# Optimization experiments

Hardware: AMD Instinct MI355X
Metric: run time of the kernel (lower is better)

## Reference

```python
import jax, jax.numpy as jnp
import numpy as np

N = 50000          # nodes
E = 800000         # edges (avg degree 16)
IN_FEATS = 128
OUT_FEATS = 64
HEADS = 4
HID = HEADS * OUT_FEATS  # 256
NEG_SLOPE = 0.2          # PyG GATConv default
EPS = 1e-5               # BatchNorm eps


def setup_inputs() -> dict:
    key = jax.random.key(0)
    ks = jax.random.split(key, 8)
    x = jax.random.normal(ks[0], (N, IN_FEATS), dtype=jnp.float32)
    edge_index = jax.random.randint(ks[1], (2, E), 0, N, dtype=jnp.int32)
    edge_attr = jax.random.normal(ks[2], (E, 8), dtype=jnp.float32)  # unused (edge_dim=None)
    # GATConv params
    W_gat = jax.random.normal(ks[3], (IN_FEATS, HEADS, OUT_FEATS), jnp.float32) * (1.0 / np.sqrt(IN_FEATS))
    att_src = jax.random.normal(ks[4], (HEADS, OUT_FEATS), jnp.float32) * 0.1
    att_dst = jax.random.normal(ks[5], (HEADS, OUT_FEATS), jnp.float32) * 0.1
    bias_gat = jnp.zeros((HID,), jnp.float32)
    # BatchNorm1 + Linear + BatchNorm2 params
    bn1_gamma = jnp.ones((HID,), jnp.float32)
    bn1_beta = jnp.zeros((HID,), jnp.float32)
    W_lin = jax.random.normal(ks[6], (HID, OUT_FEATS), jnp.float32) * (1.0 / np.sqrt(HID))
    b_lin = jnp.zeros((OUT_FEATS,), jnp.float32)
    bn2_gamma = jnp.ones((OUT_FEATS,), jnp.float32)
    bn2_beta = jnp.zeros((OUT_FEATS,), jnp.float32)
    return dict(x=x, edge_attr=edge_attr, W_gat=W_gat, att_src=att_src, att_dst=att_dst,
                bias_gat=bias_gat, bn1_gamma=bn1_gamma, bn1_beta=bn1_beta,
                W_lin=W_lin, b_lin=b_lin, bn2_gamma=bn2_gamma, bn2_beta=bn2_beta,
                edge_index=edge_index)


def _batch_norm(h, gamma, beta):
    mu = h.mean(axis=0)
    var = h.var(axis=0)
    return (h - mu) * jax.lax.rsqrt(var + EPS) * gamma + beta


def reference(x, edge_attr, W_gat, att_src, att_dst, bias_gat,
              bn1_gamma, bn1_beta, W_lin, b_lin, bn2_gamma, bn2_beta,
              edge_index):
    # --- GATConv (add_self_loops=True, edge_attr ignored since edge_dim=None) ---
    loops = jnp.arange(N, dtype=edge_index.dtype)
    src = jnp.concatenate([edge_index[0], loops])  # [E+N]
    dst = jnp.concatenate([edge_index[1], loops])
    xh = jnp.einsum('ni,iho->nho', x, W_gat)       # [N, H, O]
    a_s = (xh * att_src).sum(-1)                   # [N, H]
    a_d = (xh * att_dst).sum(-1)                   # [N, H]
    e = a_s[src] + a_d[dst]                        # [E+N, H]
    e = jnp.where(e > 0, e, NEG_SLOPE * e)         # leaky_relu
    # segment softmax over destination node
    emax = jax.ops.segment_max(e, dst, num_segments=N)        # [N, H]
    ee = jnp.exp(e - emax[dst])
    denom = jax.ops.segment_sum(ee, dst, num_segments=N)
    alpha = ee / (denom[dst] + 1e-16)              # [E+N, H]
    msg = xh[src] * alpha[:, :, None]              # [E+N, H, O]
    out = jax.ops.segment_sum(msg, dst, num_segments=N)       # [N, H, O]
    h = out.reshape(N, HID) + bias_gat             # concat heads + bias
    # --- BatchNorm + ReLU + Linear + BatchNorm + ReLU ---
    h = jax.nn.relu(_batch_norm(h, bn1_gamma, bn1_beta))
    h = h @ W_lin + b_lin
    h = jax.nn.relu(_batch_norm(h, bn2_gamma, bn2_beta))
    return h
```

## Files before the change

kernel.cpp:

```cpp
#include <hip/hip_runtime.h>
#include <hip/hip_bf16.h>

#define IN_F 128
#define HID 256
#define OUT_F 64
#define NEG 0.2f
#define CAP 64

typedef __attribute__((ext_vector_type(8))) short bf16x8;
typedef __attribute__((ext_vector_type(4))) float f32x4;

__device__ __forceinline__ float lrelu(float v) { return v > 0.f ? v : NEG * v; }
__device__ __forceinline__ float bf2f(ushort u) { return __uint_as_float((uint)u << 16); }
__device__ __forceinline__ ushort f2bf(float f) {
    uint i = __float_as_uint(f);
    i += 0x7fffu + ((i >> 16) & 1u);
    return (ushort)(i >> 16);
}

__global__ void k_init(const float* __restrict__ Wg, const float* __restrict__ Wl,
                       ushort* __restrict__ Wgt, ushort* __restrict__ Wlt,
                       int* cnt, int Nn, float* stats) {
    int i = blockIdx.x * 256 + threadIdx.x;
    if (i < Nn) cnt[i] = 0;
    if (i < 640) stats[i] = 0.f;
    if (i < IN_F * HID) {
        int c = i >> 7, k = i & 127;
        Wgt[i] = f2bf(Wg[k * HID + c]);
    }
    if (i < OUT_F * HID) {
        int c = i >> 8, k = i & 255;
        Wlt[i] = f2bf(Wl[k * OUT_F + c]);
    }
}

__global__ __launch_bounds__(256) void k_scatter(const int* __restrict__ e_src,
                                                 const int* __restrict__ e_dst, int E,
                                                 int* __restrict__ cnt, int* __restrict__ bin) {
    int e = blockIdx.x * 256 + threadIdx.x;
    if (e >= E) return;
    int d = e_dst[e];
    int pos = atomicAdd(&cnt[d], 1);
    if (pos < CAP) bin[(size_t)d * CAP + pos] = e_src[e];
}

__global__ __launch_bounds__(256) void k_gemm(const float* __restrict__ x,
                                              const ushort* __restrict__ Wgt,
                                              const float* __restrict__ att_s,
                                              const float* __restrict__ att_d,
                                              ushort* __restrict__ xhb,
                                              float* __restrict__ a_s,
                                              float* __restrict__ a_d, int Nn) {
    __shared__ ushort Alds[64][136];
    int t = threadIdx.x;
    int w = t >> 6, lane = t & 63;
    int row0 = blockIdx.x * 64;

    for (int i = t; i < 2048; i += 256) {
        int r = i >> 5, c = i & 31;
        int gr = row0 + r;
        float4 v = make_float4(0.f, 0.f, 0.f, 0.f);
        if (gr < Nn) v = *(const float4*)(x + (size_t)gr * IN_F + c * 4);
        *(ushort4*)(&Alds[r][c * 4]) = make_ushort4(f2bf(v.x), f2bf(v.y), f2bf(v.z), f2bf(v.w));
    }

    int qw = lane >> 4, lr = lane & 15;
    bf16x8 bf[4][4];
#pragma unroll
    for (int ct = 0; ct < 4; ++ct)
#pragma unroll
        for (int kt = 0; kt < 4; ++kt) {
            int col = w * 64 + ct * 16 + lr;
            bf[ct][kt] = *(const bf16x8*)(Wgt + (size_t)col * IN_F + kt * 32 + qw * 8);
        }

    f32x4 zero = {0.f, 0.f, 0.f, 0.f};
    f32x4 acc[4][4];
#pragma unroll
    for (int rt = 0; rt < 4; ++rt)
#pragma unroll
        for (int ct = 0; ct < 4; ++ct) acc[rt][ct] = zero;

    __syncthreads();
#pragma unroll
    for (int kt = 0; kt < 4; ++kt) {
#pragma unroll
        for (int rt = 0; rt < 4; ++rt) {
            bf16x8 af = *(const bf16x8*)(&Alds[rt * 16 + lr][kt * 32 + qw * 8]);
#pragma unroll
            for (int ct = 0; ct < 4; ++ct)
                acc[rt][ct] = __builtin_amdgcn_mfma_f32_16x16x32_bf16(af, bf[ct][kt], acc[rt][ct], 0, 0, 0);
        }
    }

    float asv[4], adv[4];
#pragma unroll
    for (int ct = 0; ct < 4; ++ct) {
        asv[ct] = att_s[w * 64 + ct * 16 + lr];
        adv[ct] = att_d[w * 64 + ct * 16 + lr];
    }

#pragma unroll
    for (int rt = 0; rt < 4; ++rt)
#pragma unroll
        for (int r = 0; r < 4; ++r) {
            int row = row0 + rt * 16 + qw * 4 + r;
            float ss = 0.f, dd = 0.f;
#pragma unroll
            for (int ct = 0; ct < 4; ++ct) {
                float v = acc[rt][ct][r];
                ss += v * asv[ct];
                dd += v * adv[ct];
                if (row < Nn) xhb[(size_t)row * HID + w * 64 + ct * 16 + lr] = f2bf(v);
            }
#pragma unroll
            for (int off = 1; off < 16; off <<= 1) {
                ss += __shfl_xor(ss, off);
                dd += __shfl_xor(dd, off);
            }
            if (row < Nn && lr == 0) {
                a_s[row * 4 + w] = ss;
                a_d[row * 4 + w] = dd;
            }
        }
}

__global__ __launch_bounds__(256) void k_gat(const int* __restrict__ cnt,
                                             const int* __restrict__ bin,
                                             const ushort* __restrict__ xhb,
                                             const float* __restrict__ a_s,
                                             const float* __restrict__ a_d,
                                             const float* __restrict__ bias,
                                             ushort* __restrict__ hgb, int Nn) {
    int w = threadIdx.x >> 6, lane = threadIdx.x & 63;
    int i = blockIdx.x * 4 + w;
    if (i >= Nn) return;
    int deg = cnt[i]; if (deg > CAP) deg = CAP;
    const int* colp = bin + (size_t)i * CAP;
    int q = lane >> 4, r = lane & 15;

    float adq = a_d[i * 4 + q];
    float asq = a_s[i * 4 + q];
    float ps = __expf(lrelu(asq + adq));

    ushort4 sv = *(const ushort4*)(xhb + (size_t)i * HID + lane * 4);
    float4 acc;
    acc.x = ps * bf2f(sv.x); acc.y = ps * bf2f(sv.y);
    acc.z = ps * bf2f(sv.z); acc.w = ps * bf2f(sv.w);

    float dl = 0.f;
    int c[4]; float p[4];
#pragma unroll
    for (int s = 0; s < 4; ++s) {
        int slot = s * 16 + r;
        bool valid = slot < deg;
        c[s] = valid ? colp[slot] : 0;
        float pv = 0.f;
        if (valid) pv = __expf(lrelu(a_s[c[s] * 4 + q] + adq));
        p[s] = pv;
        dl += pv;
    }
#pragma unroll
    for (int s = 0; s < 4; ++s) {
        int base = s * 16;
        if (base >= deg) break;
        int m_ = deg - base; if (m_ > 16) m_ = 16;
#pragma unroll 4
        for (int jj = 0; jj < m_; ++jj) {
            int srcl = (lane & 48) + jj;
            int cj   = __shfl(c[s], srcl);
            float pj = __shfl(p[s], srcl);
            ushort4 xv = *(const ushort4*)(xhb + (size_t)cj * HID + lane * 4);
            acc.x += pj * bf2f(xv.x);
            acc.y += pj * bf2f(xv.y);
            acc.z += pj * bf2f(xv.z);
            acc.w += pj * bf2f(xv.w);
        }
    }

#pragma unroll
    for (int off = 8; off; off >>= 1) dl += __shfl_xor(dl, off);
    float inv = 1.f / (dl + ps + 1e-16f);

    float4 b4 = *(const float4*)(bias + lane * 4);
    ushort4 o;
    o.x = f2bf(acc.x * inv + b4.x);
    o.y = f2bf(acc.y * inv + b4.y);
    o.z = f2bf(acc.z * inv + b4.z);
    o.w = f2bf(acc.w * inv + b4.w);
    *(ushort4*)(hgb + (size_t)i * HID + lane * 4) = o;
}

__global__ __launch_bounds__(256) void k_bnstat1(const ushort* __restrict__ hgb, int Nn,
                                                 float* __restrict__ sums) {
    __shared__ float sbuf[512];
    int t = threadIdx.x;
    sbuf[t] = 0.f; sbuf[t + 256] = 0.f;
    __syncthreads();
    int c0 = (t & 31) * 8;
    float s[8] = {}, sq[8] = {};
    for (int row = blockIdx.x * 8 + (t >> 5); row < Nn; row += gridDim.x * 8) {
        uint4 u = *(const uint4*)(hgb + (size_t)row * HID + c0);
        uint uu[4] = {u.x, u.y, u.z, u.w};
#pragma unroll
        for (int p = 0; p < 4; ++p) {
            float v0 = __uint_as_float(uu[p] << 16);
            float v1 = __uint_as_float(uu[p] & 0xffff0000u);
            s[p * 2] += v0;  sq[p * 2] += v0 * v0;
            s[p * 2 + 1] += v1; sq[p * 2 + 1] += v1 * v1;
        }
    }
#pragma unroll
    for (int j = 0; j < 8; ++j) {
        atomicAdd(&sbuf[c0 + j], s[j]);
        atomicAdd(&sbuf[256 + c0 + j], sq[j]);
    }
    __syncthreads();
    atomicAdd(&sums[t], sbuf[t]);
    atomicAdd(&sums[256 + t], sbuf[t + 256]);
}

__global__ __launch_bounds__(256) void k_lin(const ushort* __restrict__ hgb,
                                             const float* __restrict__ bn1s, float Ninv,
                                             const float* __restrict__ g1, const float* __restrict__ b1,
                                             const ushort* __restrict__ Wlt,
                                             const float* __restrict__ bl,
                                             ushort* __restrict__ h2b,
                                             float* __restrict__ bn2s, int Nn) {
    __shared__ ushort Alds[128][264];
    __shared__ float sc1[256], sf1[256];
    __shared__ float sbuf2[128];
    int t = threadIdx.x;
    int w = t >> 6, lane = t & 63;
    int row0 = blockIdx.x * 128;

    {
        float mu = bn1s[t] * Ninv;
        float var = bn1s[256 + t] * Ninv - mu * mu;
        float a = g1[t] * rsqrtf(var + 1e-5f);
        sc1[t] = a; sf1[t] = b1[t] - mu * a;
    }
    if (t < 128) sbuf2[t] = 0.f;
    __syncthreads();

    for (int i = t; i < 4096; i += 256) {
        int rr = i >> 5, c8 = (i & 31) * 8;
        int gr = row0 + rr;
        ushort ob[8] = {0, 0, 0, 0, 0, 0, 0, 0};
        if (gr < Nn) {
            uint4 u = *(const uint4*)(hgb + (size_t)gr * HID + c8);
            uint uu[4] = {u.x, u.y, u.z, u.w};
#pragma unroll
            for (int p = 0; p < 4; ++p) {
                float v0 = __uint_as_float(uu[p] << 16);
                float v1 = __uint_as_float(uu[p] & 0xffff0000u);
                int cA = c8 + p * 2, cB = cA + 1;
                v0 = fmaxf(v0 * sc1[cA] + sf1[cA], 0.f);
                v1 = fmaxf(v1 * sc1[cB] + sf1[cB], 0.f);
                ob[p * 2] = f2bf(v0);
                ob[p * 2 + 1] = f2bf(v1);
            }
        }
        *(ushort4*)(&Alds[rr][c8]) = make_ushort4(ob[0], ob[1], ob[2], ob[3]);
        *(ushort4*)(&Alds[rr][c8 + 4]) = make_ushort4(ob[4], ob[5], ob[6], ob[7]);
    }
    __syncthreads();

    int qw = lane >> 4, lr = lane & 15;
    f32x4 zero = {0.f, 0.f, 0.f, 0.f};
    f32x4 acc[2][4];
#pragma unroll
    for (int a = 0; a < 2; ++a)
#pragma unroll
        for (int b = 0; b < 4; ++b) acc[a][b] = zero;

#pragma unroll
    for (int kt = 0; kt < 8; ++kt) {
        bf16x8 a0 = *(const bf16x8*)(&Alds[w * 32 + lr][kt * 32 + qw * 8]);
        bf16x8 a1 = *(const bf16x8*)(&Alds[w * 32 + 16 + lr][kt * 32 + qw * 8]);
#pragma unroll
        for (int ct = 0; ct < 4; ++ct) {
            bf16x8 b = *(const bf16x8*)(Wlt + (size_t)(ct * 16 + lr) * HID + kt * 32 + qw * 8);
            acc[0][ct] = __builtin_amdgcn_mfma_f32_16x16x32_bf16(a0, b, acc[0][ct], 0, 0, 0);
            acc[1][ct] = __builtin_amdgcn_mfma_f32_16x16x32_bf16(a1, b, acc[1][ct], 0, 0, 0);
        }
    }

#pragma unroll
    for (int ct = 0; ct < 4; ++ct) {
        float blc = bl[ct * 16 + lr];
        float s2 = 0.f, q2 = 0.f;
#pragma unroll
        for (int rt = 0; rt < 2; ++rt)
#pragma unroll
            for (int r = 0; r < 4; ++r) {
                int row = row0 + w * 32 + rt * 16 + qw * 4 + r;
                if (row < Nn) {
                    ushort u = f2bf(acc[rt][ct][r] + blc);
                    h2b[(size_t)row * OUT_F + ct * 16 + lr] = u;
                    float vr = bf2f(u);
                    s2 += vr; q2 += vr * vr;
                }
            }
        atomicAdd(&sbuf2[ct * 16 + lr], s2);
        atomicAdd(&sbuf2[64 + ct * 16 + lr], q2);
    }
    __syncthreads();
    if (t < 128) atomicAdd(&bn2s[t], sbuf2[t]);
}

__global__ __launch_bounds__(256) void k_out(const ushort* __restrict__ h2b,
                                             const float* __restrict__ bn2s, float Ninv,
                                             const float* __restrict__ g2, const float* __restrict__ b2,
                                             float* __restrict__ out, int Nn) {
    __shared__ float sc[64], sf[64];
    int t = threadIdx.x;
    if (t < 64) {
        float mu = bn2s[t] * Ninv;
        float var = bn2s[64 + t] * Ninv - mu * mu;
        float a = g2[t] * rsqrtf(var + 1e-5f);
        sc[t] = a; sf[t] = b2[t] - mu * a;
    }
    __syncthreads();
    int total8 = Nn * 8;
    for (int i = blockIdx.x * 256 + t; i < total8; i += gridDim.x * 256) {
        uint4 u = ((const uint4*)h2b)[i];
        int c0 = (i & 7) * 8;
        uint uu[4] = {u.x, u.y, u.z, u.w};
        float o[8];
#pragma unroll
        for (int p = 0; p < 4; ++p) {
            float v0 = __uint_as_float(uu[p] << 16);
            float v1 = __uint_as_float(uu[p] & 0xffff0000u);
            o[p * 2] = fmaxf(v0 * sc[c0 + p * 2] + sf[c0 + p * 2], 0.f);
            o[p * 2 + 1] = fmaxf(v1 * sc[c0 + p * 2 + 1] + sf[c0 + p * 2 + 1], 0.f);
        }
        float4* op = (float4*)(out + (size_t)i * 8);
        op[0] = make_float4(o[0], o[1], o[2], o[3]);
        op[1] = make_float4(o[4], o[5], o[6], o[7]);
    }
}

extern "C" void kernel_launch(void* const* d_in, const int* in_sizes, int n_in,
                              void* d_out, int out_size, void* d_ws, size_t ws_size,
                              hipStream_t stream) {
    const float* x     = (const float*)d_in[0];
    const float* Wg    = (const float*)d_in[2];
    const float* att_s = (const float*)d_in[3];
    const float* att_d = (const float*)d_in[4];
    const float* bias_g= (const float*)d_in[5];
    const float* g1    = (const float*)d_in[6];
    const float* b1    = (const float*)d_in[7];
    const float* Wl    = (const float*)d_in[8];
    const float* bl    = (const float*)d_in[9];
    const float* g2    = (const float*)d_in[10];
    const float* b2    = (const float*)d_in[11];
    const int*   ei    = (const int*)d_in[12];

    const int N = in_sizes[0] / IN_F;
    const int E = in_sizes[12] / 2;
    const int* e_src = ei;
    const int* e_dst = ei + E;
    const int NTILES = (N + 255) / 256;

    char* wsb = (char*)d_ws;
    size_t o = 0;
    auto take = [&](size_t bytes) -> void* {
        void* p = wsb + o;
        o = (o + bytes + 255) & ~(size_t)255;
        return p;
    };
    ushort* xhb    = (ushort*)take((size_t)N * HID * 2);
    ushort* hgb    = (ushort*)take((size_t)N * HID * 2);
    ushort* h2b    = (ushort*)take((size_t)N * OUT_F * 2);
    ushort* Wgt    = (ushort*)take((size_t)IN_F * HID * 2);
    ushort* Wlt    = (ushort*)take((size_t)OUT_F * HID * 2);
    float*  a_s    = (float*)take((size_t)N * 4 * 4);
    float*  a_d    = (float*)take((size_t)N * 4 * 4);
    int*    cnt    = (int*)take((size_t)N * 4);
    int*    bin    = (int*)take((size_t)N * CAP * 4);
    float*  stats  = (float*)take(1024 * 4);
    float* bn1s = stats;
    float* bn2s = stats + 512;

    float* out = (float*)d_out;
    float Ninv = 1.0f / (float)N;

    k_init<<<NTILES, 256, 0, stream>>>(Wg, Wl, Wgt, Wlt, cnt, N, stats);
    k_scatter<<<(E + 255) / 256, 256, 0, stream>>>(e_src, e_dst, E, cnt, bin);
    k_gemm<<<(N + 63) / 64, 256, 0, stream>>>(x, Wgt, att_s, att_d, xhb, a_s, a_d, N);
    k_gat<<<(N + 3) / 4, 256, 0, stream>>>(cnt, bin, xhb, a_s, a_d, bias_g, hgb, N);
    k_bnstat1<<<256, 256, 0, stream>>>(hgb, N, bn1s);
    k_lin<<<(N + 127) / 128, 256, 0, stream>>>(hgb, bn1s, Ninv, g1, b1, Wlt, bl, h2b, bn2s, N);
    k_out<<<1024, 256, 0, stream>>>(h2b, bn2s, Ninv, g2, b2, out, N);
}
```

Before: 204.1 us.

## Split neighbors across lane quarters with wide row loads in GAT aggregation

Each wavefront now splits one destination node's neighbors across four 16-lane groups. Every lane loads 16 bf16 values (two 16-byte loads) per neighbor row and handles two neighbors per iteration, where before the whole wave walked the neighbors one at a time with 8-byte loads and shuffles. Partial accumulators and softmax denominators are combined with xor-shuffles across the lane groups, and a single quarter writes the output. This aims to raise memory-level parallelism and cut per-neighbor shuffle overhead. In exchange it costs more registers (16 accumulators), 34 cross-lane shuffles for the final reduction, and wasted lanes when the degree is not a multiple of 8.

```diff
diff --git a/kernel.cpp b/kernel.cpp
--- a/kernel.cpp
+++ b/kernel.cpp
@@ -137,58 +137,86 @@
     if (i >= Nn) return;
     int deg = cnt[i]; if (deg > CAP) deg = CAP;
     const int* colp = bin + (size_t)i * CAP;
-    int q = lane >> 4, r = lane & 15;
-
-    float adq = a_d[i * 4 + q];
-    float asq = a_s[i * 4 + q];
-    float ps = __expf(lrelu(asq + adq));
-
-    ushort4 sv = *(const ushort4*)(xhb + (size_t)i * HID + lane * 4);
-    float4 acc;
-    acc.x = ps * bf2f(sv.x); acc.y = ps * bf2f(sv.y);
-    acc.z = ps * bf2f(sv.z); acc.w = ps * bf2f(sv.w);
+    int qq = lane >> 4;
+    int r  = lane & 15;
+    int h  = r >> 2;
+
+    float adh = a_d[i * 4 + h];
+    float ash = a_s[i * 4 + h];
+    float ps = __expf(lrelu(ash + adh));
+
+    float acc[16];
+#pragma unroll
+    for (int j = 0; j < 16; ++j) acc[j] = 0.f;
+
+#define ACC8(U, P, B) \
+    acc[B+0] += (P) * __uint_as_float((U).x << 16); \
+    acc[B+1] += (P) * __uint_as_float((U).x & 0xffff0000u); \
+    acc[B+2] += (P) * __uint_as_float((U).y << 16); \
+    acc[B+3] += (P) * __uint_as_float((U).y & 0xffff0000u); \
+    acc[B+4] += (P) * __uint_as_float((U).z << 16); \
+    acc[B+5] += (P) * __uint_as_float((U).z & 0xffff0000u); \
+    acc[B+6] += (P) * __uint_as_float((U).w << 16); \
+    acc[B+7] += (P) * __uint_as_float((U).w & 0xffff0000u);
+
+    if (qq == 0) {
+        const ushort* rp = xhb + (size_t)i * HID + r * 16;
+        uint4 s0 = *(const uint4*)rp;
+        uint4 s1 = *(const uint4*)(rp + 8);
+        ACC8(s0, ps, 0)
+        ACC8(s1, ps, 8)
+    }
 
     float dl = 0.f;
-    int c[4]; float p[4];
-#pragma unroll
-    for (int s = 0; s < 4; ++s) {
-        int slot = s * 16 + r;
-        bool valid = slot < deg;
-        c[s] = valid ? colp[slot] : 0;
-        float pv = 0.f;
-        if (valid) pv = __expf(lrelu(a_s[c[s] * 4 + q] + adq));
-        p[s] = pv;
-        dl += pv;
-    }
-#pragma unroll
-    for (int s = 0; s < 4; ++s) {
-        int base = s * 16;
-        if (base >= deg) break;
-        int m_ = deg - base; if (m_ > 16) m_ = 16;
-#pragma unroll 4
-        for (int jj = 0; jj < m_; ++jj) {
-            int srcl = (lane & 48) + jj;
-            int cj   = __shfl(c[s], srcl);
-            float pj = __shfl(p[s], srcl);
-            ushort4 xv = *(const ushort4*)(xhb + (size_t)cj * HID + lane * 4);
-            acc.x += pj * bf2f(xv.x);
-            acc.y += pj * bf2f(xv.y);
-            acc.z += pj * bf2f(xv.z);
-            acc.w += pj * bf2f(xv.w);
-        }
-    }
-
-#pragma unroll
-    for (int off = 8; off; off >>= 1) dl += __shfl_xor(dl, off);
-    float inv = 1.f / (dl + ps + 1e-16f);
-
-    float4 b4 = *(const float4*)(bias + lane * 4);
-    ushort4 o;
-    o.x = f2bf(acc.x * inv + b4.x);
-    o.y = f2bf(acc.y * inv + b4.y);
-    o.z = f2bf(acc.z * inv + b4.z);
-    o.w = f2bf(acc.w * inv + b4.w);
-    *(ushort4*)(hgb + (size_t)i * HID + lane * 4) = o;
+    for (int g = 0; g < deg; g += 8) {
+        int sA = g + qq, sB = g + 4 + qq;
+        bool vA = sA < deg, vB = sB < deg;
+        int cA = colp[vA ? sA : deg - 1];
+        int cB = colp[vB ? sB : deg - 1];
+        float eA = a_s[cA * 4 + h] + adh;
+        float eB = a_s[cB * 4 + h] + adh;
+        const ushort* rpA = xhb + (size_t)cA * HID + r * 16;
+        const ushort* rpB = xhb + (size_t)cB * HID + r * 16;
+        uint4 a0 = *(const uint4*)rpA;
+        uint4 a1 = *(const uint4*)(rpA + 8);
+        uint4 b0 = *(const uint4*)rpB;
+        uint4 b1 = *(const uint4*)(rpB + 8);
+        float pA = vA ? __expf(lrelu(eA)) : 0.f;
+        float pB = vB ? __expf(lrelu(eB)) : 0.f;
+        dl += pA + pB;
+        ACC8(a0, pA, 0)
+        ACC8(a1, pA, 8)
+        ACC8(b0, pB, 0)
+        ACC8(b1, pB, 8)
+    }
+#undef ACC8
+
+#pragma unroll
+    for (int j = 0; j < 16; ++j) {
+        acc[j] += __shfl_xor(acc[j], 16);
+        acc[j] += __shfl_xor(acc[j], 32);
+    }
+    dl += __shfl_xor(dl, 16);
+    dl += __shfl_xor(dl, 32);
+
+    if (qq == 0) {
+        float inv = 1.f / (dl + ps + 1e-16f);
+        const float4* bp = (const float4*)(bias + r * 16);
+        uint ow[8];
+#pragma unroll
+        for (int pquad = 0; pquad < 4; ++pquad) {
+            float4 b4 = bp[pquad];
+            float v0 = acc[pquad * 4 + 0] * inv + b4.x;
+            float v1 = acc[pquad * 4 + 1] * inv + b4.y;
+            float v2 = acc[pquad * 4 + 2] * inv + b4.z;
+            float v3 = acc[pquad * 4 + 3] * inv + b4.w;
+            ow[pquad * 2 + 0] = (uint)f2bf(v0) | ((uint)f2bf(v1) << 16);
+            ow[pquad * 2 + 1] = (uint)f2bf(v2) | ((uint)f2bf(v3) << 16);
+        }
+        uint4* dst = (uint4*)(hgb + (size_t)i * HID + r * 16);
+        dst[0] = make_uint4(ow[0], ow[1], ow[2], ow[3]);
+        dst[1] = make_uint4(ow[4], ow[5], ow[6], ow[7]);
+    }
 }
 
 __global__ __launch_bounds__(256) void k_bnstat1(const ushort* __restrict__ hgb, int Nn,
```

Result: faster. 200.0 us (-2.0%).
